# Kernel tuning notes

Measured on AMD Instinct MI355X. Metric: run time of the kernel, lower is better.

Reference implementation:

```python
import jax, jax.numpy as jnp
import numpy as np

CONF_T = 0.9      # confidence_threshold
NMS_T = 0.4       # nms_threshold
VAR0, VAR1 = 0.1, 0.2  # variances
SCALE = 2048.0    # image size used in decode_bbox
K = 512           # fixed candidate cap for jit-friendly NMS
N = 2_097_152     # number of priors


def setup_inputs() -> dict:
    key = jax.random.key(0)
    k1, k2, k3 = jax.random.split(key, 3)
    loc = jax.random.normal(k1, (1, N, 4), dtype=jnp.float32)
    conf = jax.random.normal(k2, (1, N, 2), dtype=jnp.float32)
    priors = jax.random.uniform(k3, (N, 4), dtype=jnp.float32)  # normalized cx,cy,w,h
    return {"loc": loc, "conf": conf, "priors": priors}


def _decode(loc, priors):
    # standard SSD decode: loc [N,4], priors [N,4] (cx,cy,w,h) -> boxes [N,4] (x1,y1,x2,y2)
    cxcy = priors[:, :2] + loc[:, :2] * VAR0 * priors[:, 2:]
    wh = priors[:, 2:] * jnp.exp(loc[:, 2:] * VAR1)
    x1y1 = cxcy - wh * 0.5
    x2y2 = x1y1 + wh
    return jnp.concatenate([x1y1, x2y2], axis=-1)


def _pairwise_iou(b):
    # b: [K,4] in pixel coords; py_cpu_nms convention with +1 on widths/heights
    area = (b[:, 2] - b[:, 0] + 1.0) * (b[:, 3] - b[:, 1] + 1.0)  # [K]
    xx1 = jnp.maximum(b[:, None, 0], b[None, :, 0])
    yy1 = jnp.maximum(b[:, None, 1], b[None, :, 1])
    xx2 = jnp.minimum(b[:, None, 2], b[None, :, 2])
    yy2 = jnp.minimum(b[:, None, 3], b[None, :, 3])
    w = jnp.maximum(xx2 - xx1 + 1.0, 0.0)
    h = jnp.maximum(yy2 - yy1 + 1.0, 0.0)
    inter = w * h
    return inter / (area[:, None] + area[None, :] - inter)


def reference(loc, conf, priors):
    boxes = _decode(loc[0], priors) * SCALE                     # [N,4] pixel coords
    scores = jax.nn.softmax(conf[0], axis=-1)[:, 1]             # [N] face scores
    # threshold: invalid -> -1 so top_k pushes them to the end
    s = jnp.where(scores > CONF_T, scores, -1.0)
    top_s, idx = jax.lax.top_k(s, K)                            # sorted desc = argsort order
    cand = boxes[idx]                                           # [K,4]
    iou = _pairwise_iou(cand)                                   # [K,K]
    keep0 = top_s > 0.0                                         # only thresholded candidates
    ar = jnp.arange(K)
    def body(i, keep):
        sup = keep[i] & (iou[i] > NMS_T) & (ar > i)             # suppress lower-scored overlaps
        return keep & ~sup
    keep = jax.lax.fori_loop(0, K, body, keep0)
    dets = jnp.concatenate([cand / SCALE, top_s[:, None]], axis=-1)  # [K,5], boxes renormalized
    return jnp.where(keep[:, None], dets, 0.0)                  # zero-padded fixed-shape dets
```

## Files before the change

kernel.cpp:

```cpp
#include <hip/hip_runtime.h>
#include <stdint.h>

#define N_PRIORS 2097152
#define KTOP 512
#define NBINS 2048
#define K1BLK 2048
#define SCAP 32
#define SELCAP 2048
#define SSTASH 0.9915f
#define NSUPB 16


__device__ __forceinline__ uint64_t pack_key(float s, int idx) {
    return ((uint64_t)__float_as_uint(s) << 32) | (uint32_t)(~idx);
}

__device__ __forceinline__ float score_of(float c0, float c1) {
    #pragma clang fp contract(off)
    float m  = fmaxf(c0, c1);
    float e0 = expf(c0 - m);
    float e1 = expf(c1 - m);
    return e1 / (e0 + e1);
}

__device__ __forceinline__ int bin_of(float s) {
    #pragma clang fp contract(off)
    int b = (int)((s - 0.9f) * 20480.0f);
    return b > (NBINS - 1) ? (NBINS - 1) : b;
}

__device__ __forceinline__ uint64_t shfl_xor64(uint64_t x, int mask) {
    int lo = __shfl_xor((int)(uint32_t)x, mask, 64);
    int hi = __shfl_xor((int)(uint32_t)(x >> 32), mask, 64);
    return ((uint64_t)(uint32_t)hi << 32) | (uint32_t)lo;
}

__global__ void k1_stash(const float4* __restrict__ conf4,
                         uint32_t* __restrict__ blk_cnt,
                         uint64_t* __restrict__ stash,
                         uint32_t* __restrict__ done_g) {
    #pragma clang fp contract(off)
    __shared__ uint32_t lcnt;
    int t = threadIdx.x;
    int blk = blockIdx.x;
    if (blk == 0 && t == 0) *done_g = 0u;
    if (t == 0) lcnt = 0;
    __syncthreads();
    uint64_t* reg = stash + (size_t)blk * SCAP;
    #pragma unroll
    for (int i = 0; i < 2; ++i) {
        int f4i = blk * 512 + t + 256 * i;
        float4 c = conf4[f4i];
        float s0 = score_of(c.x, c.y);
        float s1 = score_of(c.z, c.w);
        if (s0 > SSTASH) {
            uint32_t p = atomicAdd(&lcnt, 1u);
            if (p < SCAP) reg[p] = pack_key(s0, f4i * 2);
        }
        if (s1 > SSTASH) {
            uint32_t p = atomicAdd(&lcnt, 1u);
            if (p < SCAP) reg[p] = pack_key(s1, f4i * 2 + 1);
        }
    }
    __syncthreads();
    if (t == 0) blk_cnt[blk] = (lcnt <= SCAP) ? lcnt : 0xFFFFFFFFu;
}

__launch_bounds__(1024)
__global__ void k2_fused(const float4* __restrict__ loc,
                         const float4* __restrict__ priors,
                         const float4* __restrict__ conf4,
                         const uint32_t* __restrict__ blk_cnt,
                         const uint64_t* __restrict__ stash,
                         uint32_t* done_g,
                         uint32_t* rowany_g,
                         uint64_t* supW_g,
                         float* __restrict__ out) {
    #pragma clang fp contract(off)
    __shared__ uint64_t arena[4096];
    uint64_t* sel  = arena;
    uint64_t* supW = arena;
    __shared__ uint32_t hist[NBINS];
    __shared__ float4 bpk[KTOP];
    __shared__ float  sar[KTOP], ssc[KTOP];
    __shared__ uint64_t keepw0[8];
    __shared__ uint64_t keepw[8];
    __shared__ uint32_t rowanyL[16];
    __shared__ uint32_t nselS, fbS, anyS, tailS;
    __shared__ int bmaxS;

    int tid = threadIdx.x;
    int lane = tid & 63, wv = tid >> 6;

    if (tid == 0) { nselS = 0u; fbS = 0u; bmaxS = 0; anyS = 0u; }
    __syncthreads();

    for (int b = tid; b < K1BLK; b += 1024) {
        uint32_t c = blk_cnt[b];
        if (c == 0xFFFFFFFFu) { atomicOr(&fbS, 1u); c = 0; }
        const uint64_t* regp = stash + (size_t)b * SCAP;
        for (uint32_t j = 0; j < c; ++j) {
            uint64_t k = regp[j];
            uint32_t p = atomicAdd(&nselS, 1u);
            if (p < SELCAP) sel[p] = k; else atomicOr(&fbS, 1u);
        }
    }
    __syncthreads();
    uint32_t n = nselS;
    bool fb = (fbS != 0u) || (n < KTOP) || (n > SELCAP);
    __syncthreads();

    if (fb) {
        if (tid == 0) nselS = 0u;
        for (int b = tid; b < NBINS; b += 1024) hist[b] = 0u;
        __syncthreads();
        for (int f = tid; f < N_PRIORS / 2; f += 1024) {
            float4 c = conf4[f];
            float s0 = score_of(c.x, c.y);
            float s1 = score_of(c.z, c.w);
            if (s0 > 0.9f) atomicAdd(&hist[bin_of(s0)], 1u);
            if (s1 > 0.9f) atomicAdd(&hist[bin_of(s1)], 1u);
        }
        __syncthreads();
        for (int off = 1; off < NBINS; off <<= 1) {
            int b0 = tid, b1 = tid + 1024;
            uint32_t v0 = hist[b0] + ((b0 + off < NBINS) ? hist[b0 + off] : 0u);
            uint32_t v1 = hist[b1] + ((b1 + off < NBINS) ? hist[b1 + off] : 0u);
            __syncthreads();
            hist[b0] = v0; hist[b1] = v1;
            __syncthreads();
        }
        if (hist[tid] >= KTOP) atomicMax(&bmaxS, tid);
        if (hist[tid + 1024] >= KTOP) atomicMax(&bmaxS, tid + 1024);
        __syncthreads();
        int B = bmaxS;
        for (int f = tid; f < N_PRIORS / 2; f += 1024) {
            float4 c = conf4[f];
            float s0 = score_of(c.x, c.y);
            float s1 = score_of(c.z, c.w);
            if (s0 > 0.9f && bin_of(s0) >= B) {
                uint32_t p = atomicAdd(&nselS, 1u);
                if (p < SELCAP) sel[p] = pack_key(s0, 2 * f);
            }
            if (s1 > 0.9f && bin_of(s1) >= B) {
                uint32_t p = atomicAdd(&nselS, 1u);
                if (p < SELCAP) sel[p] = pack_key(s1, 2 * f + 1);
            }
        }
        __syncthreads();
        n = nselS; if (n > SELCAP) n = SELCAP;
        __syncthreads();
    }

    int P = KTOP; while (P < (int)n) P <<= 1;
    for (int t = tid; t < P; t += 1024) if (t >= (int)n) sel[t] = 0ull;
    __syncthreads();

    uint64_t v;

    if (P <= 1024) {
        v = (tid < P) ? sel[tid] : 0ull;
        for (int k = 2; k <= P; k <<= 1) {
            for (int j = k >> 1; j >= 64; j >>= 1) {
                if (tid < P) sel[tid] = v;
                __syncthreads();
                if (tid < P) {
                    uint64_t pv = sel[tid ^ j];
                    bool wmax = (((tid & j) == 0) == ((tid & k) == 0));
                    v = wmax ? (v > pv ? v : pv) : (v < pv ? v : pv);
                }
                __syncthreads();
            }
            int j0 = (k >> 1) < 32 ? (k >> 1) : 32;
            for (int j = j0; j >= 1; j >>= 1) {
                uint64_t pv = shfl_xor64(v, j);
                bool wmax = (((tid & j) == 0) == ((tid & k) == 0));
                v = wmax ? (v > pv ? v : pv) : (v < pv ? v : pv);
            }
        }
    } else {
        for (int k = 2; k <= P; k <<= 1) {
            for (int j = k >> 1; j > 0; j >>= 1) {
                for (int t = tid; t < P; t += 1024) {
                    int ixj = t ^ j;
                    if (ixj > t) {
                        uint64_t a = sel[t], b = sel[ixj];
                        bool sw = ((t & k) == 0) ? (a < b) : (a > b);
                        if (sw) { sel[t] = b; sel[ixj] = a; }
                    }
                }
                __syncthreads();
            }
        }
        v = (tid < KTOP) ? sel[tid] : 0ull;
    }

    {
        uint64_t key = (tid < KTOP) ? v : 0ull;
        if (tid < KTOP) {
            float4 bb; float area, sc;
            if (key != 0ull) {
                sc = __uint_as_float((uint32_t)(key >> 32));
                int idx  = (int)(~(uint32_t)key);
                float4 l = loc[idx];
                float4 p = priors[idx];
                float cx = p.x + (l.x * 0.1f) * p.z;
                float cy = p.y + (l.y * 0.1f) * p.w;
                float w  = p.z * expf(l.z * 0.2f);
                float h  = p.w * expf(l.w * 0.2f);
                float x1 = cx - w * 0.5f;
                float y1 = cy - h * 0.5f;
                float x2 = x1 + w;
                float y2 = y1 + h;
                x1 *= 2048.0f; y1 *= 2048.0f; x2 *= 2048.0f; y2 *= 2048.0f;
                bb = make_float4(x1, y1, x2, y2);
                area = (x2 - x1 + 1.0f) * (y2 - y1 + 1.0f);
            } else {
                bb = make_float4(0.f, 0.f, 0.f, 0.f); area = 1.f; sc = 0.f;
            }
            bpk[tid] = bb; sar[tid] = area; ssc[tid] = sc;
        }
        uint64_t vb = __ballot(key != 0ull);
        if (lane == 0 && wv < 8) keepw0[wv] = vb;
    }
    __syncthreads();

    {
        float4 cb0 = bpk[lane +   0], cb1 = bpk[lane +  64];
        float4 cb2 = bpk[lane + 128], cb3 = bpk[lane + 192];
        float4 cb4 = bpk[lane + 256], cb5 = bpk[lane + 320];
        float4 cb6 = bpk[lane + 384], cb7 = bpk[lane + 448];
        float ca0 = (cb0.z - cb0.x + 1.0f) * (cb0.w - cb0.y + 1.0f);
        float ca1 = (cb1.z - cb1.x + 1.0f) * (cb1.w - cb1.y + 1.0f);
        float ca2 = (cb2.z - cb2.x + 1.0f) * (cb2.w - cb2.y + 1.0f);
        float ca3 = (cb3.z - cb3.x + 1.0f) * (cb3.w - cb3.y + 1.0f);
        float ca4 = (cb4.z - cb4.x + 1.0f) * (cb4.w - cb4.y + 1.0f);
        float ca5 = (cb5.z - cb5.x + 1.0f) * (cb5.w - cb5.y + 1.0f);
        float ca6 = (cb6.z - cb6.x + 1.0f) * (cb6.w - cb6.y + 1.0f);
        float ca7 = (cb7.z - cb7.x + 1.0f) * (cb7.w - cb7.y + 1.0f);
        #define SUPC(c, CB, CA) do { \
            float xx1 = fmaxf(rb.x, CB.x); float yy1 = fmaxf(rb.y, CB.y); \
            float xx2 = fminf(rb.z, CB.z); float yy2 = fminf(rb.w, CB.w); \
            float ww = fmaxf(xx2 - xx1 + 1.0f, 0.0f); \
            float hh = fmaxf(yy2 - yy1 + 1.0f, 0.0f); \
            float inter = ww * hh; \
            float iou = inter / (ra + (CA) - inter); \
            uint64_t wrd = __ballot(iou > 0.4f && (64 * (c) + lane) > r); \
            if (lane == 0) supW_g[r * 8 + (c)] = wrd; \
            any |= wrd; } while (0)
        uint32_t mybits = 0u;
        int rbase = blockIdx.x * 32 + wv * 2;
        for (int rr = 0; rr < 2; ++rr) {
            int r = rbase + rr;
            float4 rb = bpk[r];
            float ra = sar[r];
            uint64_t any = 0ull;
            SUPC(0, cb0, ca0); SUPC(1, cb1, ca1); SUPC(2, cb2, ca2); SUPC(3, cb3, ca3);
            SUPC(4, cb4, ca4); SUPC(5, cb5, ca5); SUPC(6, cb6, ca6); SUPC(7, cb7, ca7);
            if (lane == 0 && any != 0ull) mybits |= 1u << (r & 31);
        }
        #undef SUPC
        if (lane == 0 && mybits != 0u) atomicOr(&anyS, mybits);
    }
    __syncthreads();

    if (tid == 0) {
        rowany_g[blockIdx.x] = anyS;
        __threadfence();
        uint32_t old = atomicAdd(done_g, 1u);
        tailS = (old == (uint32_t)(NSUPB - 1)) ? 1u : 0u;
    }
    __syncthreads();
    if (tailS == 0u) return;

    __threadfence();
    for (int i = tid; i < KTOP * 8; i += 1024)
        supW[i] = __hip_atomic_load(&supW_g[i], __ATOMIC_RELAXED,
                                    __HIP_MEMORY_SCOPE_AGENT);
    if (tid < 16)
        rowanyL[tid] = __hip_atomic_load(&rowany_g[tid], __ATOMIC_RELAXED,
                                         __HIP_MEMORY_SCOPE_AGENT);
    __syncthreads();

    if (tid == 0) {
        #define RA64(c) (((uint64_t)rowanyL[2*(c)]) | (((uint64_t)rowanyL[2*(c)+1]) << 32))
        uint64_t kp0 = keepw0[0], kp1 = keepw0[1], kp2 = keepw0[2], kp3 = keepw0[3];
        uint64_t kp4 = keepw0[4], kp5 = keepw0[5], kp6 = keepw0[6], kp7 = keepw0[7];
        #define APPLYROW(i) do { const uint64_t* rp = supW + (size_t)(i) * 8; \
            kp0 &= ~rp[0]; kp1 &= ~rp[1]; kp2 &= ~rp[2]; kp3 &= ~rp[3]; \
            kp4 &= ~rp[4]; kp5 &= ~rp[5]; kp6 &= ~rp[6]; kp7 &= ~rp[7]; } while (0)
        #define CHUNK(c, KPC) do { uint64_t ra = RA64(c); uint64_t m = (KPC) & ra; \
            while (m) { int b = __builtin_ctzll(m); APPLYROW((c) * 64 + b); \
                uint64_t above = (b == 63) ? 0ull : (~0ull << (b + 1)); \
                m = (KPC) & ra & above; } } while (0)
        CHUNK(0, kp0); CHUNK(1, kp1); CHUNK(2, kp2); CHUNK(3, kp3);
        CHUNK(4, kp4); CHUNK(5, kp5); CHUNK(6, kp6); CHUNK(7, kp7);
        keepw[0] = kp0; keepw[1] = kp1; keepw[2] = kp2; keepw[3] = kp3;
        keepw[4] = kp4; keepw[5] = kp5; keepw[6] = kp6; keepw[7] = kp7;
        #undef CHUNK
        #undef APPLYROW
        #undef RA64
    }
    __syncthreads();

    if (tid < KTOP) {
        const float inv = 1.0f / 2048.0f;
        int kb = (int)((keepw[tid >> 6] >> (tid & 63)) & 1ull);
        float4 bb = bpk[tid];
        float* o = out + tid * 5;
        if (kb) {
            o[0] = bb.x * inv;
            o[1] = bb.y * inv;
            o[2] = bb.z * inv;
            o[3] = bb.w * inv;
            o[4] = ssc[tid];
        } else {
            o[0] = 0.f; o[1] = 0.f; o[2] = 0.f; o[3] = 0.f; o[4] = 0.f;
        }
    }
}

extern "C" void kernel_launch(void* const* d_in, const int* in_sizes, int n_in,
                              void* d_out, int out_size, void* d_ws, size_t ws_size,
                              hipStream_t stream) {
    const float* loc    = (const float*)d_in[0];
    const float* conf   = (const float*)d_in[1];
    const float* priors = (const float*)d_in[2];
    float* out = (float*)d_out;

    uint8_t* ws = (uint8_t*)d_ws;
    uint32_t* blk_cnt  = (uint32_t*)ws;
    uint64_t* stash    = (uint64_t*)(ws + 8192);
    uint32_t* done_g   = (uint32_t*)(ws + 532480);
    uint32_t* rowany_g = (uint32_t*)(ws + 532544);
    uint64_t* supW_g   = (uint64_t*)(ws + 532608);

    k1_stash<<<K1BLK, 256, 0, stream>>>((const float4*)conf, blk_cnt, stash, done_g);
    k2_fused<<<NSUPB, 1024, 0, stream>>>((const float4*)loc, (const float4*)priors,
                                         (const float4*)conf, blk_cnt, stash,
                                         done_g, rowany_g, supW_g, out);
}
```

Measured before the change: 134.1 us.

## Compact candidates globally in stash kernel and precompute decoded boxes there

The first kernel now appends each candidate that passes the stash threshold to one global list through a global atomic counter. It also decodes that candidate's box from loc and priors right away, so the second kernel no longer walks 2048 per-block stash regions with shared atomics. The bitonic sort carries a slot index alongside each key, so the precomputed box can be fetched after sorting instead of gathering loc and priors again. The cost is contended global atomics, an extra memset launch, and extra shared traffic in the sort for the slot array.

```diff
diff --git a/kernel.cpp b/kernel.cpp
--- a/kernel.cpp
+++ b/kernel.cpp
@@ -5,7 +5,6 @@
 #define KTOP 512
 #define NBINS 2048
 #define K1BLK 2048
-#define SCAP 32
 #define SELCAP 2048
 #define SSTASH 0.9915f
 #define NSUPB 16
@@ -35,43 +34,58 @@
     return ((uint64_t)(uint32_t)hi << 32) | (uint32_t)lo;
 }
 
+__device__ __forceinline__ void emit_cand(float s, int idx,
+                                          const float4* __restrict__ loc,
+                                          const float4* __restrict__ priors,
+                                          uint64_t* __restrict__ keys_g,
+                                          float4* __restrict__ bbs_g,
+                                          uint32_t* __restrict__ nsel_g) {
+    #pragma clang fp contract(off)
+    uint32_t p = atomicAdd(nsel_g, 1u);
+    if (p < SELCAP) {
+        keys_g[p] = pack_key(s, idx);
+        float4 l  = loc[idx];
+        float4 pr = priors[idx];
+        float cx = pr.x + (l.x * 0.1f) * pr.z;
+        float cy = pr.y + (l.y * 0.1f) * pr.w;
+        float w  = pr.z * expf(l.z * 0.2f);
+        float h  = pr.w * expf(l.w * 0.2f);
+        float x1 = cx - w * 0.5f;
+        float y1 = cy - h * 0.5f;
+        float x2 = x1 + w;
+        float y2 = y1 + h;
+        x1 *= 2048.0f; y1 *= 2048.0f; x2 *= 2048.0f; y2 *= 2048.0f;
+        bbs_g[p] = make_float4(x1, y1, x2, y2);
+    }
+}
+
 __global__ void k1_stash(const float4* __restrict__ conf4,
-                         uint32_t* __restrict__ blk_cnt,
-                         uint64_t* __restrict__ stash,
-                         uint32_t* __restrict__ done_g) {
-    #pragma clang fp contract(off)
-    __shared__ uint32_t lcnt;
+                         const float4* __restrict__ loc,
+                         const float4* __restrict__ priors,
+                         uint64_t* __restrict__ keys_g,
+                         float4* __restrict__ bbs_g,
+                         uint32_t* __restrict__ nsel_g) {
+    #pragma clang fp contract(off)
     int t = threadIdx.x;
     int blk = blockIdx.x;
-    if (blk == 0 && t == 0) *done_g = 0u;
-    if (t == 0) lcnt = 0;
-    __syncthreads();
-    uint64_t* reg = stash + (size_t)blk * SCAP;
     #pragma unroll
     for (int i = 0; i < 2; ++i) {
         int f4i = blk * 512 + t + 256 * i;
         float4 c = conf4[f4i];
         float s0 = score_of(c.x, c.y);
         float s1 = score_of(c.z, c.w);
-        if (s0 > SSTASH) {
-            uint32_t p = atomicAdd(&lcnt, 1u);
-            if (p < SCAP) reg[p] = pack_key(s0, f4i * 2);
-        }
-        if (s1 > SSTASH) {
-            uint32_t p = atomicAdd(&lcnt, 1u);
-            if (p < SCAP) reg[p] = pack_key(s1, f4i * 2 + 1);
-        }
-    }
-    __syncthreads();
-    if (t == 0) blk_cnt[blk] = (lcnt <= SCAP) ? lcnt : 0xFFFFFFFFu;
+        if (s0 > SSTASH) emit_cand(s0, f4i * 2,     loc, priors, keys_g, bbs_g, nsel_g);
+        if (s1 > SSTASH) emit_cand(s1, f4i * 2 + 1, loc, priors, keys_g, bbs_g, nsel_g);
+    }
 }
 
 __launch_bounds__(1024)
 __global__ void k2_fused(const float4* __restrict__ loc,
                          const float4* __restrict__ priors,
                          const float4* __restrict__ conf4,
-                         const uint32_t* __restrict__ blk_cnt,
-                         const uint64_t* __restrict__ stash,
+                         const uint32_t* __restrict__ nsel_g,
+                         const uint64_t* __restrict__ keys_g,
+                         const float4* __restrict__ bbs_g,
                          uint32_t* done_g,
                          uint32_t* rowany_g,
                          uint64_t* supW_g,
@@ -79,6 +93,7 @@
     #pragma clang fp contract(off)
     __shared__ uint64_t arena[4096];
     uint64_t* sel  = arena;
+    uint32_t* slt  = (uint32_t*)(arena + 2048);
     uint64_t* supW = arena;
     __shared__ uint32_t hist[NBINS];
     __shared__ float4 bpk[KTOP];
@@ -86,31 +101,23 @@
     __shared__ uint64_t keepw0[8];
     __shared__ uint64_t keepw[8];
     __shared__ uint32_t rowanyL[16];
-    __shared__ uint32_t nselS, fbS, anyS, tailS;
+    __shared__ uint32_t nselS, anyS, tailS;
     __shared__ int bmaxS;
 
     int tid = threadIdx.x;
     int lane = tid & 63, wv = tid >> 6;
 
-    if (tid == 0) { nselS = 0u; fbS = 0u; bmaxS = 0; anyS = 0u; }
-    __syncthreads();
-
-    for (int b = tid; b < K1BLK; b += 1024) {
-        uint32_t c = blk_cnt[b];
-        if (c == 0xFFFFFFFFu) { atomicOr(&fbS, 1u); c = 0; }
-        const uint64_t* regp = stash + (size_t)b * SCAP;
-        for (uint32_t j = 0; j < c; ++j) {
-            uint64_t k = regp[j];
-            uint32_t p = atomicAdd(&nselS, 1u);
-            if (p < SELCAP) sel[p] = k; else atomicOr(&fbS, 1u);
-        }
-    }
-    __syncthreads();
-    uint32_t n = nselS;
-    bool fb = (fbS != 0u) || (n < KTOP) || (n > SELCAP);
-    __syncthreads();
-
-    if (fb) {
+    if (tid == 0) { anyS = 0u; bmaxS = 0; }
+
+    uint32_t n = *nsel_g;
+    bool fb = (n < KTOP) || (n > SELCAP);
+
+    if (!fb) {
+        for (int t = tid; t < (int)n; t += 1024) {
+            sel[t] = keys_g[t];
+            slt[t] = (uint32_t)t;
+        }
+    } else {
         if (tid == 0) nselS = 0u;
         for (int b = tid; b < NBINS; b += 1024) hist[b] = 0u;
         __syncthreads();
@@ -149,33 +156,40 @@
         }
         __syncthreads();
         n = nselS; if (n > SELCAP) n = SELCAP;
-        __syncthreads();
-    }
+    }
+    __syncthreads();
 
     int P = KTOP; while (P < (int)n) P <<= 1;
-    for (int t = tid; t < P; t += 1024) if (t >= (int)n) sel[t] = 0ull;
+    for (int t = tid; t < P; t += 1024)
+        if (t >= (int)n) { sel[t] = 0ull; slt[t] = 0u; }
     __syncthreads();
 
     uint64_t v;
+    uint32_t sl;
 
     if (P <= 1024) {
-        v = (tid < P) ? sel[tid] : 0ull;
+        v  = (tid < P) ? sel[tid] : 0ull;
+        sl = (tid < P) ? slt[tid] : 0u;
         for (int k = 2; k <= P; k <<= 1) {
             for (int j = k >> 1; j >= 64; j >>= 1) {
-                if (tid < P) sel[tid] = v;
+                if (tid < P) { sel[tid] = v; slt[tid] = sl; }
                 __syncthreads();
                 if (tid < P) {
                     uint64_t pv = sel[tid ^ j];
+                    uint32_t ps = slt[tid ^ j];
                     bool wmax = (((tid & j) == 0) == ((tid & k) == 0));
-                    v = wmax ? (v > pv ? v : pv) : (v < pv ? v : pv);
+                    bool take = wmax ? (pv > v) : (pv < v);
+                    if (take) { v = pv; sl = ps; }
                 }
                 __syncthreads();
             }
             int j0 = (k >> 1) < 32 ? (k >> 1) : 32;
             for (int j = j0; j >= 1; j >>= 1) {
                 uint64_t pv = shfl_xor64(v, j);
+                uint32_t ps = (uint32_t)__shfl_xor((int)sl, j, 64);
                 bool wmax = (((tid & j) == 0) == ((tid & k) == 0));
-                v = wmax ? (v > pv ? v : pv) : (v < pv ? v : pv);
+                bool take = wmax ? (pv > v) : (pv < v);
+                v = take ? pv : v; sl = take ? ps : sl;
             }
         }
     } else {
@@ -186,13 +200,17 @@
                     if (ixj > t) {
                         uint64_t a = sel[t], b = sel[ixj];
                         bool sw = ((t & k) == 0) ? (a < b) : (a > b);
-                        if (sw) { sel[t] = b; sel[ixj] = a; }
+                        if (sw) {
+                            sel[t] = b; sel[ixj] = a;
+                            uint32_t sa = slt[t]; slt[t] = slt[ixj]; slt[ixj] = sa;
+                        }
                     }
                 }
                 __syncthreads();
             }
         }
-        v = (tid < KTOP) ? sel[tid] : 0ull;
+        v  = (tid < KTOP) ? sel[tid] : 0ull;
+        sl = (tid < KTOP) ? slt[tid] : 0u;
     }
 
     {
@@ -201,20 +219,24 @@
             float4 bb; float area, sc;
             if (key != 0ull) {
                 sc = __uint_as_float((uint32_t)(key >> 32));
-                int idx  = (int)(~(uint32_t)key);
-                float4 l = loc[idx];
-                float4 p = priors[idx];
-                float cx = p.x + (l.x * 0.1f) * p.z;
-                float cy = p.y + (l.y * 0.1f) * p.w;
-                float w  = p.z * expf(l.z * 0.2f);
-                float h  = p.w * expf(l.w * 0.2f);
-                float x1 = cx - w * 0.5f;
-                float y1 = cy - h * 0.5f;
-                float x2 = x1 + w;
-                float y2 = y1 + h;
-                x1 *= 2048.0f; y1 *= 2048.0f; x2 *= 2048.0f; y2 *= 2048.0f;
-                bb = make_float4(x1, y1, x2, y2);
-                area = (x2 - x1 + 1.0f) * (y2 - y1 + 1.0f);
+                if (!fb) {
+                    bb = bbs_g[sl];
+                } else {
+                    int idx  = (int)(~(uint32_t)key);
+                    float4 l = loc[idx];
+                    float4 p = priors[idx];
+                    float cx = p.x + (l.x * 0.1f) * p.z;
+                    float cy = p.y + (l.y * 0.1f) * p.w;
+                    float w  = p.z * expf(l.z * 0.2f);
+                    float h  = p.w * expf(l.w * 0.2f);
+                    float x1 = cx - w * 0.5f;
+                    float y1 = cy - h * 0.5f;
+                    float x2 = x1 + w;
+                    float y2 = y1 + h;
+                    x1 *= 2048.0f; y1 *= 2048.0f; x2 *= 2048.0f; y2 *= 2048.0f;
+                    bb = make_float4(x1, y1, x2, y2);
+                }
+                area = (bb.z - bb.x + 1.0f) * (bb.w - bb.y + 1.0f);
             } else {
                 bb = make_float4(0.f, 0.f, 0.f, 0.f); area = 1.f; sc = 0.f;
             }
@@ -329,14 +351,19 @@
     float* out = (float*)d_out;
 
     uint8_t* ws = (uint8_t*)d_ws;
-    uint32_t* blk_cnt  = (uint32_t*)ws;
-    uint64_t* stash    = (uint64_t*)(ws + 8192);
-    uint32_t* done_g   = (uint32_t*)(ws + 532480);
-    uint32_t* rowany_g = (uint32_t*)(ws + 532544);
-    uint64_t* supW_g   = (uint64_t*)(ws + 532608);
-
-    k1_stash<<<K1BLK, 256, 0, stream>>>((const float4*)conf, blk_cnt, stash, done_g);
+    uint32_t* nsel_g   = (uint32_t*)ws;
+    uint32_t* done_g   = (uint32_t*)(ws + 4);
+    uint32_t* rowany_g = (uint32_t*)(ws + 128);
+    uint64_t* keys_g   = (uint64_t*)(ws + 256);
+    float4*   bbs_g    = (float4*)(ws + 16640);
+    uint64_t* supW_g   = (uint64_t*)(ws + 49408);
+
+    hipMemsetAsync(ws, 0, 8, stream);
+    k1_stash<<<K1BLK, 256, 0, stream>>>((const float4*)conf,
+                                        (const float4*)loc,
+                                        (const float4*)priors,
+                                        keys_g, bbs_g, nsel_g);
     k2_fused<<<NSUPB, 1024, 0, stream>>>((const float4*)loc, (const float4*)priors,
-                                         (const float4*)conf, blk_cnt, stash,
+                                         (const float4*)conf, nsel_g, keys_g, bbs_g,
                                          done_g, rowany_g, supW_g, out);
 }
```

Measured after the change: 142.2 us. 1.06x slower.

## Decode candidate boxes in stash kernel and carry slot indices through sort

Applied to the files above, without the earlier changes.

The first kernel now decodes boxes for stashed candidates while they are being stashed and writes them to a workspace box stash. The fused kernel loads those boxes into shared memory and carries a slot index alongside each key through the bitonic sort, so the top-K gather reads from LDS instead of doing dependent global loads of loc and priors. The stash gather also reserves space with one atomic per block instead of one per element. The cost is a larger box-stash write in the first kernel, an extra 32 KB of LDS, and extra shuffles and stores in the sort, which could lower occupancy or add sort overhead.

```diff
diff --git a/kernel.cpp b/kernel.cpp
--- a/kernel.cpp
+++ b/kernel.cpp
@@ -35,9 +35,30 @@
     return ((uint64_t)(uint32_t)hi << 32) | (uint32_t)lo;
 }
 
+__device__ __forceinline__ float4 decode_box(int idx,
+                                             const float4* __restrict__ loc,
+                                             const float4* __restrict__ priors) {
+    #pragma clang fp contract(off)
+    float4 l = loc[idx];
+    float4 p = priors[idx];
+    float cx = p.x + (l.x * 0.1f) * p.z;
+    float cy = p.y + (l.y * 0.1f) * p.w;
+    float w  = p.z * expf(l.z * 0.2f);
+    float h  = p.w * expf(l.w * 0.2f);
+    float x1 = cx - w * 0.5f;
+    float y1 = cy - h * 0.5f;
+    float x2 = x1 + w;
+    float y2 = y1 + h;
+    x1 *= 2048.0f; y1 *= 2048.0f; x2 *= 2048.0f; y2 *= 2048.0f;
+    return make_float4(x1, y1, x2, y2);
+}
+
 __global__ void k1_stash(const float4* __restrict__ conf4,
+                         const float4* __restrict__ loc,
+                         const float4* __restrict__ priors,
                          uint32_t* __restrict__ blk_cnt,
-                         uint64_t* __restrict__ stash,
+                         uint64_t* __restrict__ key_stash,
+                         float4* __restrict__ box_stash,
                          uint32_t* __restrict__ done_g) {
     #pragma clang fp contract(off)
     __shared__ uint32_t lcnt;
@@ -46,7 +67,8 @@
     if (blk == 0 && t == 0) *done_g = 0u;
     if (t == 0) lcnt = 0;
     __syncthreads();
-    uint64_t* reg = stash + (size_t)blk * SCAP;
+    uint64_t* kreg = key_stash + (size_t)blk * SCAP;
+    float4*   breg = box_stash + (size_t)blk * SCAP;
     #pragma unroll
     for (int i = 0; i < 2; ++i) {
         int f4i = blk * 512 + t + 256 * i;
@@ -55,11 +77,17 @@
         float s1 = score_of(c.z, c.w);
         if (s0 > SSTASH) {
             uint32_t p = atomicAdd(&lcnt, 1u);
-            if (p < SCAP) reg[p] = pack_key(s0, f4i * 2);
+            if (p < SCAP) {
+                kreg[p] = pack_key(s0, f4i * 2);
+                breg[p] = decode_box(f4i * 2, loc, priors);
+            }
         }
         if (s1 > SSTASH) {
             uint32_t p = atomicAdd(&lcnt, 1u);
-            if (p < SCAP) reg[p] = pack_key(s1, f4i * 2 + 1);
+            if (p < SCAP) {
+                kreg[p] = pack_key(s1, f4i * 2 + 1);
+                breg[p] = decode_box(f4i * 2 + 1, loc, priors);
+            }
         }
     }
     __syncthreads();
@@ -71,7 +99,8 @@
                          const float4* __restrict__ priors,
                          const float4* __restrict__ conf4,
                          const uint32_t* __restrict__ blk_cnt,
-                         const uint64_t* __restrict__ stash,
+                         const uint64_t* __restrict__ key_stash,
+                         const float4* __restrict__ box_stash,
                          uint32_t* done_g,
                          uint32_t* rowany_g,
                          uint64_t* supW_g,
@@ -79,7 +108,9 @@
     #pragma clang fp contract(off)
     __shared__ uint64_t arena[4096];
     uint64_t* sel  = arena;
+    uint32_t* slt  = (uint32_t*)(arena + 2048);
     uint64_t* supW = arena;
+    __shared__ float4 bbxL[SELCAP];
     __shared__ uint32_t hist[NBINS];
     __shared__ float4 bpk[KTOP];
     __shared__ float  sar[KTOP], ssc[KTOP];
@@ -92,17 +123,23 @@
     int tid = threadIdx.x;
     int lane = tid & 63, wv = tid >> 6;
 
-    if (tid == 0) { nselS = 0u; fbS = 0u; bmaxS = 0; anyS = 0u; }
+    if (tid == 0) { nselS = 0u; fbS = 0u; anyS = 0u; bmaxS = 0; }
     __syncthreads();
 
     for (int b = tid; b < K1BLK; b += 1024) {
         uint32_t c = blk_cnt[b];
         if (c == 0xFFFFFFFFu) { atomicOr(&fbS, 1u); c = 0; }
-        const uint64_t* regp = stash + (size_t)b * SCAP;
+        uint32_t base = 0;
+        if (c > 0) base = atomicAdd(&nselS, c);
         for (uint32_t j = 0; j < c; ++j) {
-            uint64_t k = regp[j];
-            uint32_t p = atomicAdd(&nselS, 1u);
-            if (p < SELCAP) sel[p] = k; else atomicOr(&fbS, 1u);
+            uint32_t p = base + j;
+            if (p < SELCAP) {
+                sel[p]  = key_stash[(size_t)b * SCAP + j];
+                bbxL[p] = box_stash[(size_t)b * SCAP + j];
+                slt[p]  = p;
+            } else {
+                atomicOr(&fbS, 1u);
+            }
         }
     }
     __syncthreads();
@@ -140,11 +177,11 @@
             float s1 = score_of(c.z, c.w);
             if (s0 > 0.9f && bin_of(s0) >= B) {
                 uint32_t p = atomicAdd(&nselS, 1u);
-                if (p < SELCAP) sel[p] = pack_key(s0, 2 * f);
+                if (p < SELCAP) { sel[p] = pack_key(s0, 2 * f); slt[p] = p; }
             }
             if (s1 > 0.9f && bin_of(s1) >= B) {
                 uint32_t p = atomicAdd(&nselS, 1u);
-                if (p < SELCAP) sel[p] = pack_key(s1, 2 * f + 1);
+                if (p < SELCAP) { sel[p] = pack_key(s1, 2 * f + 1); slt[p] = p; }
             }
         }
         __syncthreads();
@@ -153,29 +190,36 @@
     }
 
     int P = KTOP; while (P < (int)n) P <<= 1;
-    for (int t = tid; t < P; t += 1024) if (t >= (int)n) sel[t] = 0ull;
+    for (int t = tid; t < P; t += 1024)
+        if (t >= (int)n) { sel[t] = 0ull; slt[t] = 0u; }
     __syncthreads();
 
     uint64_t v;
+    uint32_t sl;
 
     if (P <= 1024) {
-        v = (tid < P) ? sel[tid] : 0ull;
+        v  = (tid < P) ? sel[tid] : 0ull;
+        sl = (tid < P) ? slt[tid] : 0u;
         for (int k = 2; k <= P; k <<= 1) {
             for (int j = k >> 1; j >= 64; j >>= 1) {
-                if (tid < P) sel[tid] = v;
+                if (tid < P) { sel[tid] = v; slt[tid] = sl; }
                 __syncthreads();
                 if (tid < P) {
                     uint64_t pv = sel[tid ^ j];
+                    uint32_t ps = slt[tid ^ j];
                     bool wmax = (((tid & j) == 0) == ((tid & k) == 0));
-                    v = wmax ? (v > pv ? v : pv) : (v < pv ? v : pv);
+                    bool take = wmax ? (pv > v) : (pv < v);
+                    if (take) { v = pv; sl = ps; }
                 }
                 __syncthreads();
             }
             int j0 = (k >> 1) < 32 ? (k >> 1) : 32;
             for (int j = j0; j >= 1; j >>= 1) {
                 uint64_t pv = shfl_xor64(v, j);
+                uint32_t ps = (uint32_t)__shfl_xor((int)sl, j, 64);
                 bool wmax = (((tid & j) == 0) == ((tid & k) == 0));
-                v = wmax ? (v > pv ? v : pv) : (v < pv ? v : pv);
+                bool take = wmax ? (pv > v) : (pv < v);
+                v = take ? pv : v; sl = take ? ps : sl;
             }
         }
     } else {
@@ -186,13 +230,17 @@
                     if (ixj > t) {
                         uint64_t a = sel[t], b = sel[ixj];
                         bool sw = ((t & k) == 0) ? (a < b) : (a > b);
-                        if (sw) { sel[t] = b; sel[ixj] = a; }
+                        if (sw) {
+                            sel[t] = b; sel[ixj] = a;
+                            uint32_t sa = slt[t]; slt[t] = slt[ixj]; slt[ixj] = sa;
+                        }
                     }
                 }
                 __syncthreads();
             }
         }
-        v = (tid < KTOP) ? sel[tid] : 0ull;
+        v  = (tid < KTOP) ? sel[tid] : 0ull;
+        sl = (tid < KTOP) ? slt[tid] : 0u;
     }
 
     {
@@ -201,20 +249,13 @@
             float4 bb; float area, sc;
             if (key != 0ull) {
                 sc = __uint_as_float((uint32_t)(key >> 32));
-                int idx  = (int)(~(uint32_t)key);
-                float4 l = loc[idx];
-                float4 p = priors[idx];
-                float cx = p.x + (l.x * 0.1f) * p.z;
-                float cy = p.y + (l.y * 0.1f) * p.w;
-                float w  = p.z * expf(l.z * 0.2f);
-                float h  = p.w * expf(l.w * 0.2f);
-                float x1 = cx - w * 0.5f;
-                float y1 = cy - h * 0.5f;
-                float x2 = x1 + w;
-                float y2 = y1 + h;
-                x1 *= 2048.0f; y1 *= 2048.0f; x2 *= 2048.0f; y2 *= 2048.0f;
-                bb = make_float4(x1, y1, x2, y2);
-                area = (x2 - x1 + 1.0f) * (y2 - y1 + 1.0f);
+                if (!fb) {
+                    bb = bbxL[sl];
+                } else {
+                    int idx = (int)(~(uint32_t)key);
+                    bb = decode_box(idx, loc, priors);
+                }
+                area = (bb.z - bb.x + 1.0f) * (bb.w - bb.y + 1.0f);
             } else {
                 bb = make_float4(0.f, 0.f, 0.f, 0.f); area = 1.f; sc = 0.f;
             }
@@ -329,14 +370,19 @@
     float* out = (float*)d_out;
 
     uint8_t* ws = (uint8_t*)d_ws;
-    uint32_t* blk_cnt  = (uint32_t*)ws;
-    uint64_t* stash    = (uint64_t*)(ws + 8192);
-    uint32_t* done_g   = (uint32_t*)(ws + 532480);
-    uint32_t* rowany_g = (uint32_t*)(ws + 532544);
-    uint64_t* supW_g   = (uint64_t*)(ws + 532608);
-
-    k1_stash<<<K1BLK, 256, 0, stream>>>((const float4*)conf, blk_cnt, stash, done_g);
+    uint32_t* blk_cnt   = (uint32_t*)ws;
+    uint64_t* key_stash = (uint64_t*)(ws + 8192);
+    float4*   box_stash = (float4*)(ws + 532480);
+    uint32_t* done_g    = (uint32_t*)(ws + 1581056);
+    uint32_t* rowany_g  = (uint32_t*)(ws + 1581120);
+    uint64_t* supW_g    = (uint64_t*)(ws + 1581184);
+
+    k1_stash<<<K1BLK, 256, 0, stream>>>((const float4*)conf,
+                                        (const float4*)loc,
+                                        (const float4*)priors,
+                                        blk_cnt, key_stash, box_stash, done_g);
     k2_fused<<<NSUPB, 1024, 0, stream>>>((const float4*)loc, (const float4*)priors,
-                                         (const float4*)conf, blk_cnt, stash,
+                                         (const float4*)conf, blk_cnt,
+                                         key_stash, box_stash,
                                          done_g, rowany_g, supW_g, out);
 }
```

After: 140.0 us. +4.4%, slower.
